# Optimization experiments

Measured on AMD Instinct MI355X. Metric: run time of the kernel, lower is better.

## Reference

```python
import jax, jax.numpy as jnp
import numpy as np

NUM_TYPES = 8
NUM_REL = 6
N_LAYERS = 2


def setup_inputs() -> dict:
    key = jax.random.key(0)
    ks = jax.random.split(key, 8)
    N, E, D_in, D = 20000, 320000, 512, 256
    node_feature = jax.random.normal(ks[0], (N, D_in), dtype=jnp.float32)
    node_type = jax.random.randint(ks[1], (N,), 0, NUM_TYPES)
    edge_index = jax.random.randint(ks[2], (2, E), 0, N)
    edge_type = jax.random.randint(ks[3], (E,), 0, NUM_REL)
    node_position = jnp.arange(N)
    # learned params
    adapt_W = jax.random.normal(ks[4], (NUM_TYPES, D, D_in), dtype=jnp.float32) * 0.02
    adapt_b = jnp.zeros((NUM_TYPES, D), dtype=jnp.float32)
    W_rel = jax.random.normal(ks[5], (N_LAYERS, NUM_REL, D, D), dtype=jnp.float32) * 0.05
    W_self = jax.random.normal(ks[6], (N_LAYERS, D, D), dtype=jnp.float32) * 0.05
    b_self = jnp.zeros((N_LAYERS, D), dtype=jnp.float32)
    return {
        "node_feature": node_feature,
        "node_type": node_type,
        "edge_index": edge_index,
        "edge_type": edge_type,
        "node_position": node_position,
        "adapt_W": adapt_W,
        "adapt_b": adapt_b,
        "W_rel": W_rel,
        "W_self": W_self,
        "b_self": b_self,
    }


def reference(node_feature, node_type, edge_index, edge_type, node_position,
              adapt_W, adapt_b, W_rel, W_self, b_self):
    N = node_feature.shape[0]
    D = adapt_W.shape[1]
    # per-node-type adaptation: res[i] = tanh(W_{t_i} x_i + b_{t_i})
    # (original loops over types with boolean gather/scatter; here we mask-select)
    h = jnp.zeros((N, D), dtype=node_feature.dtype)
    for t in range(NUM_TYPES):
        y = jnp.tanh(node_feature @ adapt_W[t].T + adapt_b[t])
        h = jnp.where((node_type == t)[:, None], y, h)
    # dropout p=0.0 -> identity
    src, dst = edge_index[0], edge_index[1]
    deg = jax.ops.segment_sum(jnp.ones(src.shape, h.dtype), dst, num_segments=N)
    inv_deg = (1.0 / jnp.maximum(deg, 1.0))[:, None]  # [N,1]
    # relational GNN layer stack (stand-in for unseen GraphConv)
    for l in range(N_LAYERS):
        hr = jnp.einsum('nd,rde->rne', h, W_rel[l])      # [R,N,D]
        msg = hr[edge_type, src]                          # [E,D] gather by (relation, src)
        agg = jax.ops.segment_sum(msg, dst, num_segments=N)
        h = jax.nn.relu(agg * inv_deg + h @ W_self[l] + b_self[l])
    return h
```

## Files before the change

kernel.cpp:

```cpp
#include <hip/hip_runtime.h>

constexpr int NTYPES = 8;
constexpr int NREL   = 6;
constexpr int NSLOT  = 7;
constexpr int D      = 256;
constexpr int DIN    = 512;
constexpr int LDH    = NSLOT * D;

using short8 = __attribute__((ext_vector_type(8))) short;
using f32x4  = __attribute__((ext_vector_type(4))) float;

__device__ __forceinline__ ushort f2b(float f) {
  unsigned u = __float_as_uint(f);
  u += 0x7fffu + ((u >> 16) & 1u);
  return (ushort)(u >> 16);
}
__device__ __forceinline__ float b2f(unsigned bits16) {
  return __uint_as_float(bits16 << 16);
}

#define GLOAD_LDS16(g, l)                                              \
  __builtin_amdgcn_global_load_lds(                                    \
      (__attribute__((address_space(1))) void*)(g),                    \
      (__attribute__((address_space(3))) void*)(l), 16, 0, 0)

__global__ void k_prep_fused(int* __restrict__ deg,
                             const float* __restrict__ X, ushort* __restrict__ Xb,
                             const float* __restrict__ Wa, ushort* __restrict__ Wab,
                             const float* __restrict__ Wrel, const float* __restrict__ Wself,
                             ushort* __restrict__ Wcat,
                             int N, int nz, int nx, int nw, int n4x, int n4w) {
  const int b = blockIdx.x;
  const int tid = threadIdx.x;
  if (b < nz) {
    int i = b * 256 + tid;
    if (i < N) deg[i] = 0;
  } else if (b < nz + nx) {
    int i = (b - nz) * 256 + tid;
    if (i < n4x) {
      float4 v = ((const float4*)X)[i];
      ushort4 o; o.x = f2b(v.x); o.y = f2b(v.y); o.z = f2b(v.z); o.w = f2b(v.w);
      ((ushort4*)Xb)[i] = o;
    }
  } else if (b < nz + nx + nw) {
    int i = (b - nz - nx) * 256 + tid;
    if (i < n4w) {
      float4 v = ((const float4*)Wa)[i];
      ushort4 o; o.x = f2b(v.x); o.y = f2b(v.y); o.z = f2b(v.z); o.w = f2b(v.w);
      ((ushort4*)Wab)[i] = o;
    }
  } else {
    int local = b - nz - nx - nw;
    int l = local / (NSLOT * 256);
    int s = (local % (NSLOT * 256)) / 256;
    int o = (local % 256) * 256 + tid;
    int e = o >> 8, d = o & 255;
    float v = (s < NREL) ? Wrel[(((size_t)l * NREL + s) * D + d) * D + e]
                         : Wself[((size_t)l * D + d) * D + e];
    Wcat[(((size_t)l * NSLOT + s) * D + e) * D + d] = f2b(v);
  }
}

__global__ void k_count_fused(const int* __restrict__ ntype, int* __restrict__ blockcnt,
                              const int* __restrict__ dst, int* __restrict__ deg,
                              int N, int E, int nbN) {
  __shared__ int cnt[NTYPES];
  const int b = blockIdx.x;
  if (b < nbN) {
    int i = b * 256 + threadIdx.x;
    if (threadIdx.x < NTYPES) cnt[threadIdx.x] = 0;
    __syncthreads();
    int t = (i < N) ? ntype[i] : -1;
#pragma unroll
    for (int ty = 0; ty < NTYPES; ++ty) {
      unsigned long long m = __ballot(t == ty);
      if ((threadIdx.x & 63) == 0 && m) atomicAdd(&cnt[ty], __popcll(m));
    }
    __syncthreads();
    if (threadIdx.x < NTYPES) blockcnt[b * NTYPES + threadIdx.x] = cnt[threadIdx.x];
  } else {
    int e = (b - nbN) * 256 + threadIdx.x;
    if (e < E) atomicAdd(&deg[dst[e]], 1);
  }
}

__global__ __launch_bounds__(512)
void k_type_scan(const int* __restrict__ blockcnt, int* __restrict__ boffset,
                 int* __restrict__ cnt, int* __restrict__ offt, int nb) {
  __shared__ int tot[NTYPES];
  __shared__ int base[NTYPES];
  const int w = threadIdx.x >> 6;
  const int l = threadIdx.x & 63;
  int v0 = (l < nb) ? blockcnt[l * NTYPES + w] : 0;
  int v1 = (64 + l < nb) ? blockcnt[(64 + l) * NTYPES + w] : 0;
  int s0 = v0;
#pragma unroll
  for (int o = 1; o < 64; o <<= 1) { int t = __shfl_up(s0, o); if (l >= o) s0 += t; }
  int total0 = __shfl(s0, 63);
  int s1 = v1;
#pragma unroll
  for (int o = 1; o < 64; o <<= 1) { int t = __shfl_up(s1, o); if (l >= o) s1 += t; }
  s1 += total0;
  int totalw = __shfl(s1, 63);
  if (l == 0) { tot[w] = totalw; cnt[w] = totalw; }
  __syncthreads();
  if (threadIdx.x == 0) {
    int s = 0;
    for (int ty = 0; ty < NTYPES; ++ty) { base[ty] = s; offt[ty] = s; s += tot[ty]; }
  }
  __syncthreads();
  const int bs = base[w];
  if (l < nb) boffset[l * NTYPES + w] = bs + s0 - v0;
  if (64 + l < nb) boffset[(64 + l) * NTYPES + w] = bs + s1 - v1;
}

__global__ void k_scatter_scan(const int* __restrict__ ntype, const int* __restrict__ boffset,
                               int* __restrict__ perm,
                               const int* __restrict__ deg, int* __restrict__ rowptr,
                               int* __restrict__ bsum, int N, int nbN) {
  __shared__ int sm[256];
  const int b = blockIdx.x;
  if (b < nbN) {
    int i = b * 256 + threadIdx.x;
    if (threadIdx.x < NTYPES) sm[threadIdx.x] = boffset[b * NTYPES + threadIdx.x];
    __syncthreads();
    int t = (i < N) ? ntype[i] : -1;
    int lane = threadIdx.x & 63;
#pragma unroll
    for (int ty = 0; ty < NTYPES; ++ty) {
      unsigned long long m = __ballot(t == ty);
      if (m) {
        int wbase = 0;
        if (lane == 0) wbase = atomicAdd(&sm[ty], __popcll(m));
        wbase = __shfl(wbase, 0);
        if (t == ty) {
          int rank = __popcll(m & ((1ull << lane) - 1ull));
          perm[wbase + rank] = i;
        }
      }
    }
  } else {
    const int bb = b - nbN;
    int i = bb * 256 + threadIdx.x;
    int v = (i < N) ? deg[i] : 0;
    sm[threadIdx.x] = v;
    __syncthreads();
    for (int o = 1; o < 256; o <<= 1) {
      int t = (threadIdx.x >= o) ? sm[threadIdx.x - o] : 0;
      __syncthreads();
      sm[threadIdx.x] += t;
      __syncthreads();
    }
    if (i < N) rowptr[i] = sm[threadIdx.x] - v;
    if (threadIdx.x == 255) bsum[bb] = sm[255];
  }
}

__global__ __launch_bounds__(64)
void k_scan_bsum(int* __restrict__ bsum, int nb) {
  const int l = threadIdx.x;
  int v0 = (l < nb) ? bsum[l] : 0;
  int v1 = (64 + l < nb) ? bsum[64 + l] : 0;
  int s0 = v0;
#pragma unroll
  for (int o = 1; o < 64; o <<= 1) { int t = __shfl_up(s0, o); if (l >= o) s0 += t; }
  int total0 = __shfl(s0, 63);
  int s1 = v1;
#pragma unroll
  for (int o = 1; o < 64; o <<= 1) { int t = __shfl_up(s1, o); if (l >= o) s1 += t; }
  s1 += total0;
  if (l < nb) bsum[l] = s0 - v0;
  if (64 + l < nb) bsum[64 + l] = s1 - v1;
}

__global__ void k_scan_add(int* __restrict__ rowptr, int* __restrict__ cursor,
                           const int* __restrict__ bsum, const int* __restrict__ deg,
                           float* __restrict__ inv, int N, int E) {
  int i = blockIdx.x * 256 + threadIdx.x;
  if (i < N) {
    int r = rowptr[i] + bsum[blockIdx.x];
    rowptr[i] = r;
    cursor[i] = r;
    inv[i] = 1.0f / fmaxf((float)deg[i], 1.0f);
  }
  if (i == 0) rowptr[N] = E;
}
__global__ void k_sortedges(const int* __restrict__ src, const int* __restrict__ dst,
                            const int* __restrict__ et, int* cursor,
                            int* __restrict__ epack, int E) {
  int e = blockIdx.x * 256 + threadIdx.x;
  if (e < E) {
    int pos = atomicAdd(&cursor[dst[e]], 1);
    epack[pos] = (src[e] << 3) | et[e];
  }
}

template <int BM, int BN, int NTN, int KDIM, bool ADAPT, int OCC>
__global__ __launch_bounds__(256, OCC)
void k_mfma_gemm(const ushort* __restrict__ A, const ushort* __restrict__ B,
                 const float* __restrict__ bias,
                 const int* __restrict__ perm, const int* __restrict__ cnt,
                 const int* __restrict__ off,
                 ushort* __restrict__ Cout, int N, int ldC) {
  const int nwg = gridDim.x;
  const int qq = nwg >> 3, rr = nwg & 7;
  const int xcd = blockIdx.x & 7, idx = blockIdx.x >> 3;
  const int wgid = (xcd < rr ? xcd * (qq + 1) : rr * (qq + 1) + (xcd - rr) * qq) + idx;

  int mcnt = N, mtile, ntile;
  const int* permt = nullptr;
  const ushort* Bt = B;
  const float* biast = bias;
  if (ADAPT) {
    const int mt = nwg / (NTYPES * NTN);
    const int t = wgid / (mt * NTN);
    const int rem = wgid % (mt * NTN);
    mtile = rem / NTN;
    ntile = rem % NTN;
    mcnt = cnt[t];
    permt = perm + off[t];
    Bt = B + (size_t)t * D * KDIM;
    biast = bias + t * D;
  } else {
    mtile = wgid / NTN;
    ntile = wgid % NTN;
  }
  const int m0 = mtile * BM;
  if (m0 >= mcnt) return;
  const int n0 = ntile * BN;

  __shared__ ushort SM[3][2][BM * 32];
  static_assert(BM * BN <= 3 * 2 * BM * 32, "C tile must fit in staging LDS");

  const int tid  = threadIdx.x;
  const int lane = tid & 63;
  const int w    = tid >> 6;
  constexpr int FR = BM / 32;
  constexpr int FC = BN / 32;
  const int wr   = (w >> 1) * (BM / 2);
  const int wc   = (w & 1) * (BN / 2);

  constexpr int PW = BM / 16 / 4;
  const ushort* gA[PW];
  const ushort* gB[PW];
  int lo[PW];
#pragma unroll
  for (int u = 0; u < PW; ++u) {
    const int c  = w + u * 4;
    const int r  = c * 16 + (lane >> 2);
    const int sl = (lane & 3) ^ ((r >> 1) & 3);
    int ga;
    if (ADAPT) ga = permt[min(m0 + r, mcnt - 1)];
    else       ga = min(m0 + r, N - 1);
    gA[u] = A + (size_t)ga * KDIM + sl * 8;
    gB[u] = Bt + (size_t)(n0 + r) * KDIM + sl * 8;
    lo[u] = c * 512;
  }

  auto STAGE = [&](int k0, int buf) {
#pragma unroll
    for (int u = 0; u < PW; ++u) {
      GLOAD_LDS16(gA[u] + k0, &SM[buf][0][lo[u]]);
      GLOAD_LDS16(gB[u] + k0, &SM[buf][1][lo[u]]);
    }
  };
  auto WAIT_LPS = [&]() {
    if constexpr (PW == 1) asm volatile("s_waitcnt vmcnt(2)" ::: "memory");
    else                   asm volatile("s_waitcnt vmcnt(4)" ::: "memory");
  };

  f32x4 acc[FR][FC] = {};
  const int r15 = lane & 15;
  const int g   = lane >> 4;
  const int gsw = g ^ ((r15 >> 1) & 3);

  auto COMPUTE = [&](int buf) {
    short8 af[FR], bf[FC];
#pragma unroll
    for (int i = 0; i < FR; ++i)
      af[i] = *(const short8*)(&SM[buf][0][(wr + i * 16 + r15) * 32 + gsw * 8]);
#pragma unroll
    for (int j = 0; j < FC; ++j)
      bf[j] = *(const short8*)(&SM[buf][1][(wc + j * 16 + r15) * 32 + gsw * 8]);
#pragma unroll
    for (int i = 0; i < FR; ++i)
#pragma unroll
      for (int j = 0; j < FC; ++j)
        acc[i][j] = __builtin_amdgcn_mfma_f32_16x16x32_bf16(af[i], bf[j], acc[i][j], 0, 0, 0);
  };

  constexpr int NT = KDIM / 32;
  static_assert(NT >= 3, "pipeline needs NT >= 3");

  STAGE(0, 0);
  STAGE(32, 1);

#pragma unroll
  for (int kt = 0; kt < NT - 1; ++kt) {
    WAIT_LPS();
    __builtin_amdgcn_s_barrier();
    __builtin_amdgcn_sched_barrier(0);
    COMPUTE(kt % 3);
    if (kt + 2 < NT) STAGE((kt + 2) * 32, (kt + 2) % 3);
  }
  asm volatile("s_waitcnt vmcnt(0)" ::: "memory");
  __builtin_amdgcn_s_barrier();
  __builtin_amdgcn_sched_barrier(0);
  COMPUTE((NT - 1) % 3);

  __syncthreads();
  ushort* Ct = (ushort*)SM;
#pragma unroll
  for (int i = 0; i < FR; ++i) {
#pragma unroll
    for (int q4 = 0; q4 < 4; ++q4) {
      const int row = wr + i * 16 + (lane >> 4) * 4 + q4;
#pragma unroll
      for (int j = 0; j < FC; ++j) {
        const int col = wc + j * 16 + r15;
        float v = acc[i][j][q4];
        if (ADAPT) v = tanhf(v + biast[n0 + col]);
        Ct[row * BN + col] = f2b(v);
      }
    }
  }
  __syncthreads();
  constexpr int C8 = BN / 8;
  constexpr int UNITS = BM * C8;
#pragma unroll
  for (int u0 = 0; u0 < UNITS; u0 += 256) {
    const int u = u0 + tid;
    const int row = u / C8, c8 = u % C8;
    const int rl = m0 + row;
    if (rl < mcnt) {
      const int grow = ADAPT ? permt[rl] : rl;
      *(short8*)(Cout + (size_t)grow * ldC + n0 + c8 * 8) =
          *(const short8*)(Ct + row * BN + c8 * 8);
    }
  }
}

template <bool LAST>
__global__ void k_combine(const ushort* __restrict__ Hall, const int* __restrict__ rowptr,
                          const int* __restrict__ epack, const float* __restrict__ invd,
                          const float* __restrict__ bias, void* __restrict__ outp, int N) {
  int v = blockIdx.x * 4 + (threadIdx.x >> 6);
  if (v >= N) return;
  int lane = threadIdx.x & 63;
  int e0 = rowptr[v], e1 = rowptr[v + 1];
  const uint2 s = *(const uint2*)(Hall + (size_t)v * LDH + NREL * D + lane * 4);
  float iv = invd[v];
  const float4 b4 = *(const float4*)(bias + lane * 4);

  float a0 = 0.f, a1 = 0.f, a2 = 0.f, a3 = 0.f;
  int e = e0;
  for (; e + 8 <= e1; e += 8) {
    uint2 u[8];
#pragma unroll
    for (int k = 0; k < 8; ++k) {
      int p = epack[e + k];
      u[k] = *(const uint2*)(Hall + (size_t)(p >> 3) * LDH + (p & 7) * D + lane * 4);
    }
#pragma unroll
    for (int k = 0; k < 8; ++k) {
      a0 += b2f(u[k].x & 0xffffu);
      a1 += __uint_as_float(u[k].x & 0xffff0000u);
      a2 += b2f(u[k].y & 0xffffu);
      a3 += __uint_as_float(u[k].y & 0xffff0000u);
    }
  }
  if (e + 4 <= e1) {
    uint2 u[4];
#pragma unroll
    for (int k = 0; k < 4; ++k) {
      int p = epack[e + k];
      u[k] = *(const uint2*)(Hall + (size_t)(p >> 3) * LDH + (p & 7) * D + lane * 4);
    }
#pragma unroll
    for (int k = 0; k < 4; ++k) {
      a0 += b2f(u[k].x & 0xffffu);
      a1 += __uint_as_float(u[k].x & 0xffff0000u);
      a2 += b2f(u[k].y & 0xffffu);
      a3 += __uint_as_float(u[k].y & 0xffff0000u);
    }
    e += 4;
  }
  for (; e < e1; ++e) {
    int p = epack[e];
    const uint2 u = *(const uint2*)(Hall + (size_t)(p >> 3) * LDH + (p & 7) * D + lane * 4);
    a0 += b2f(u.x & 0xffffu);
    a1 += __uint_as_float(u.x & 0xffff0000u);
    a2 += b2f(u.y & 0xffffu);
    a3 += __uint_as_float(u.y & 0xffff0000u);
  }
  float o0 = fmaxf(fmaf(a0, iv, b2f(s.x & 0xffffu)) + b4.x, 0.f);
  float o1 = fmaxf(fmaf(a1, iv, __uint_as_float(s.x & 0xffff0000u)) + b4.y, 0.f);
  float o2 = fmaxf(fmaf(a2, iv, b2f(s.y & 0xffffu)) + b4.z, 0.f);
  float o3 = fmaxf(fmaf(a3, iv, __uint_as_float(s.y & 0xffff0000u)) + b4.w, 0.f);
  if (LAST) {
    float4 o; o.x = o0; o.y = o1; o.z = o2; o.w = o3;
    ((float4*)outp)[(size_t)v * 64 + lane] = o;
  } else {
    ushort4 o; o.x = f2b(o0); o.y = f2b(o1); o.z = f2b(o2); o.w = f2b(o3);
    ((ushort4*)outp)[(size_t)v * 64 + lane] = o;
  }
}

extern "C" void kernel_launch(void* const* d_in, const int* in_sizes, int n_in,
                              void* d_out, int out_size, void* d_ws, size_t ws_size,
                              hipStream_t stream) {
  const float* X       = (const float*)d_in[0];
  const int*   ntype   = (const int*)d_in[1];
  const int*   eidx    = (const int*)d_in[2];
  const int*   etype   = (const int*)d_in[3];
  const float* adapt_W = (const float*)d_in[5];
  const float* adapt_b = (const float*)d_in[6];
  const float* W_rel   = (const float*)d_in[7];
  const float* W_self  = (const float*)d_in[8];
  const float* b_self  = (const float*)d_in[9];

  const int N = in_sizes[1];
  const int E = in_sizes[3];
  const int* src = eidx;
  const int* dst = eidx + E;

  char* ws = (char*)d_ws;
  size_t o = 0;
  auto alloc = [&](size_t bytes) { void* p = ws + o; o += (bytes + 255) & ~255ull; return p; };

  ushort* Hall  = (ushort*)alloc((size_t)N * LDH * 2);
  ushort* Xb    = Hall;
  ushort* h     = (ushort*)alloc((size_t)N * D * 2);
  ushort* Wab   = (ushort*)alloc((size_t)NTYPES * D * DIN * 2);
  ushort* Wcat  = (ushort*)alloc((size_t)2 * NSLOT * D * D * 2);
  int*   deg    = (int*)alloc((size_t)N * 4);
  float* inv    = (float*)alloc((size_t)N * 4);
  int*   perm   = (int*)alloc((size_t)N * 4);
  int*   rowptr = (int*)alloc((size_t)(N + 1) * 4);
  int*   cursor = (int*)alloc((size_t)N * 4);
  int*   epack  = (int*)alloc((size_t)E * 4);
  int*   bsum   = (int*)alloc(1024 * 4);
  int*   blockcnt = (int*)alloc((size_t)1024 * NTYPES * 4);
  int*   boffset  = (int*)alloc((size_t)1024 * NTYPES * 4);
  int*   cnt    = (int*)alloc(NTYPES * 4);
  int*   offt   = (int*)alloc(NTYPES * 4);

  const int thr = 256;
  const int nbN = (N + thr - 1) / thr;
  const int nbE = (E + thr - 1) / thr;

  const int n4x = N * DIN / 4;
  const int n4w = NTYPES * D * DIN / 4;
  const int nz = nbN;
  const int nx = (n4x + thr - 1) / thr;
  const int nw = (n4w + thr - 1) / thr;
  const int np = 2 * NSLOT * (D * D / 256);
  k_prep_fused<<<nz + nx + nw + np, thr, 0, stream>>>(deg, X, Xb, adapt_W, Wab,
                                                      W_rel, W_self, Wcat,
                                                      N, nz, nx, nw, n4x, n4w);

  k_count_fused<<<nbN + nbE, thr, 0, stream>>>(ntype, blockcnt, dst, deg, N, E, nbN);
  k_type_scan<<<1, 512, 0, stream>>>(blockcnt, boffset, cnt, offt, nbN);
  k_scatter_scan<<<2 * nbN, thr, 0, stream>>>(ntype, boffset, perm, deg, rowptr, bsum, N, nbN);
  k_scan_bsum<<<1, 64, 0, stream>>>(bsum, nbN);
  k_scan_add<<<nbN, 256, 0, stream>>>(rowptr, cursor, bsum, deg, inv, N, E);
  k_sortedges<<<nbE, 256, 0, stream>>>(src, dst, etype, cursor, epack, E);

  const int mtA = (N + 63) / 64;
  const int nwgA = NTYPES * mtA * (D / 64);
  k_mfma_gemm<64, 64, D / 64, DIN, true, 6><<<nwgA, 256, 0, stream>>>(
      Xb, Wab, adapt_b, perm, cnt, offt, h, N, D);

  const int mtL = (N + 127) / 128;
  const int nwgL = mtL * (LDH / 128);
  for (int l = 0; l < 2; ++l) {
    const ushort* Wl = Wcat + (size_t)l * NSLOT * D * D;
    k_mfma_gemm<128, 128, LDH / 128, D, false, 4><<<nwgL, 256, 0, stream>>>(
        h, Wl, nullptr, nullptr, nullptr, nullptr, Hall, N, LDH);
    if (l == 0)
      k_combine<false><<<(N + 3) / 4, 256, 0, stream>>>(Hall, rowptr, epack, inv,
                                                        b_self + (size_t)l * D, h, N);
    else
      k_combine<true><<<(N + 3) / 4, 256, 0, stream>>>(Hall, rowptr, epack, inv,
                                                       b_self + (size_t)l * D, d_out, N);
  }
}
```

Baseline: 191.5 us.

## Merge preprocessing kernels and fold edge sort into adaptation GEMM launch

Cuts the preprocessing chain from seven launches to five. Type counting and degree atomics move into the conversion kernel, the type scan and a 512-wide degree scan share one launch, and the block-sum scan rides on the scatter kernel. The edge bucketing runs as extra blocks appended to the adaptation GEMM grid, so it overlaps with the matrix work. The GEMM now takes its tile count as an argument, and a separate zeroing kernel resets the degree counts before the fused kernel. The point is to remove launch gaps and serial dependencies between small kernels, at the cost of mixing atomic-heavy blocks into the GEMM grid.

New measurement: 187.5 us, median of 4. -2.0%, faster.

```diff
diff --git a/kernel.cpp b/kernel.cpp
--- a/kernel.cpp
+++ b/kernel.cpp
@@ -24,33 +24,38 @@
       (__attribute__((address_space(1))) void*)(g),                    \
       (__attribute__((address_space(3))) void*)(l), 16, 0, 0)
 
-__global__ void k_prep_fused(int* __restrict__ deg,
-                             const float* __restrict__ X, ushort* __restrict__ Xb,
-                             const float* __restrict__ Wa, ushort* __restrict__ Wab,
-                             const float* __restrict__ Wrel, const float* __restrict__ Wself,
-                             ushort* __restrict__ Wcat,
-                             int N, int nz, int nx, int nw, int n4x, int n4w) {
+__global__ void k_zero(int* __restrict__ p, int n) {
+  int i = blockIdx.x * blockDim.x + threadIdx.x;
+  if (i < n) p[i] = 0;
+}
+
+__global__ void k_prep_mega(const float* __restrict__ X, ushort* __restrict__ Xb,
+                            const float* __restrict__ Wa, ushort* __restrict__ Wab,
+                            const float* __restrict__ Wrel, const float* __restrict__ Wself,
+                            ushort* __restrict__ Wcat,
+                            const int* __restrict__ ntype, int* __restrict__ blockcnt,
+                            const int* __restrict__ dst, int* __restrict__ deg,
+                            int N, int E, int nx, int nw, int np, int nbN,
+                            int n4x, int n4w) {
+  __shared__ int cnt[NTYPES];
   const int b = blockIdx.x;
   const int tid = threadIdx.x;
-  if (b < nz) {
+  if (b < nx) {
     int i = b * 256 + tid;
-    if (i < N) deg[i] = 0;
-  } else if (b < nz + nx) {
-    int i = (b - nz) * 256 + tid;
     if (i < n4x) {
       float4 v = ((const float4*)X)[i];
       ushort4 o; o.x = f2b(v.x); o.y = f2b(v.y); o.z = f2b(v.z); o.w = f2b(v.w);
       ((ushort4*)Xb)[i] = o;
     }
-  } else if (b < nz + nx + nw) {
-    int i = (b - nz - nx) * 256 + tid;
+  } else if (b < nx + nw) {
+    int i = (b - nx) * 256 + tid;
     if (i < n4w) {
       float4 v = ((const float4*)Wa)[i];
       ushort4 o; o.x = f2b(v.x); o.y = f2b(v.y); o.z = f2b(v.z); o.w = f2b(v.w);
       ((ushort4*)Wab)[i] = o;
     }
-  } else {
-    int local = b - nz - nx - nw;
+  } else if (b < nx + nw + np) {
+    int local = b - nx - nw;
     int l = local / (NSLOT * 256);
     int s = (local % (NSLOT * 256)) / 256;
     int o = (local % 256) * 256 + tid;
@@ -58,71 +63,83 @@
     float v = (s < NREL) ? Wrel[(((size_t)l * NREL + s) * D + d) * D + e]
                          : Wself[((size_t)l * D + d) * D + e];
     Wcat[(((size_t)l * NSLOT + s) * D + e) * D + d] = f2b(v);
-  }
-}
-
-__global__ void k_count_fused(const int* __restrict__ ntype, int* __restrict__ blockcnt,
-                              const int* __restrict__ dst, int* __restrict__ deg,
-                              int N, int E, int nbN) {
-  __shared__ int cnt[NTYPES];
+  } else if (b < nx + nw + np + nbN) {
+    const int bb = b - nx - nw - np;
+    int i = bb * 256 + tid;
+    if (tid < NTYPES) cnt[tid] = 0;
+    __syncthreads();
+    int t = (i < N) ? ntype[i] : -1;
+#pragma unroll
+    for (int ty = 0; ty < NTYPES; ++ty) {
+      unsigned long long m = __ballot(t == ty);
+      if ((tid & 63) == 0 && m) atomicAdd(&cnt[ty], __popcll(m));
+    }
+    __syncthreads();
+    if (tid < NTYPES) blockcnt[bb * NTYPES + tid] = cnt[tid];
+  } else {
+    int e = (b - nx - nw - np - nbN) * 256 + tid;
+    if (e < E) atomicAdd(&deg[dst[e]], 1);
+  }
+}
+
+__global__ __launch_bounds__(512)
+void k_scan2(const int* __restrict__ blockcnt, int* __restrict__ boffset,
+             int* __restrict__ cnt, int* __restrict__ offt, int nbN,
+             const int* __restrict__ deg, int* __restrict__ rowptr,
+             int* __restrict__ bsum, int N) {
+  if (blockIdx.x == 0) {
+    __shared__ int tot[NTYPES];
+    __shared__ int base[NTYPES];
+    const int w = threadIdx.x >> 6;
+    const int l = threadIdx.x & 63;
+    int v0 = (l < nbN) ? blockcnt[l * NTYPES + w] : 0;
+    int v1 = (64 + l < nbN) ? blockcnt[(64 + l) * NTYPES + w] : 0;
+    int s0 = v0;
+#pragma unroll
+    for (int o = 1; o < 64; o <<= 1) { int t = __shfl_up(s0, o); if (l >= o) s0 += t; }
+    int total0 = __shfl(s0, 63);
+    int s1 = v1;
+#pragma unroll
+    for (int o = 1; o < 64; o <<= 1) { int t = __shfl_up(s1, o); if (l >= o) s1 += t; }
+    s1 += total0;
+    int totalw = __shfl(s1, 63);
+    if (l == 0) { tot[w] = totalw; cnt[w] = totalw; }
+    __syncthreads();
+    if (threadIdx.x == 0) {
+      int s = 0;
+      for (int ty = 0; ty < NTYPES; ++ty) { base[ty] = s; offt[ty] = s; s += tot[ty]; }
+    }
+    __syncthreads();
+    const int bs = base[w];
+    if (l < nbN) boffset[l * NTYPES + w] = bs + s0 - v0;
+    if (64 + l < nbN) boffset[(64 + l) * NTYPES + w] = bs + s1 - v1;
+  } else {
+    __shared__ int sm[512];
+    const int bb = blockIdx.x - 1;
+    const int t = threadIdx.x;
+    int i = bb * 512 + t;
+    int v = (i < N) ? deg[i] : 0;
+    sm[t] = v;
+    __syncthreads();
+    for (int o = 1; o < 512; o <<= 1) {
+      int x = (t >= o) ? sm[t - o] : 0;
+      __syncthreads();
+      sm[t] += x;
+      __syncthreads();
+    }
+    if (i < N) rowptr[i] = sm[t] - v;
+    if (t == 511) bsum[bb] = sm[511];
+  }
+}
+
+__global__ void k_scatter_bsum(const int* __restrict__ ntype, const int* __restrict__ boffset,
+                               int* __restrict__ perm, int N, int nbN,
+                               int* __restrict__ bsum, int nbs) {
+  __shared__ int cur[NTYPES];
   const int b = blockIdx.x;
   if (b < nbN) {
     int i = b * 256 + threadIdx.x;
-    if (threadIdx.x < NTYPES) cnt[threadIdx.x] = 0;
-    __syncthreads();
-    int t = (i < N) ? ntype[i] : -1;
-#pragma unroll
-    for (int ty = 0; ty < NTYPES; ++ty) {
-      unsigned long long m = __ballot(t == ty);
-      if ((threadIdx.x & 63) == 0 && m) atomicAdd(&cnt[ty], __popcll(m));
-    }
-    __syncthreads();
-    if (threadIdx.x < NTYPES) blockcnt[b * NTYPES + threadIdx.x] = cnt[threadIdx.x];
-  } else {
-    int e = (b - nbN) * 256 + threadIdx.x;
-    if (e < E) atomicAdd(&deg[dst[e]], 1);
-  }
-}
-
-__global__ __launch_bounds__(512)
-void k_type_scan(const int* __restrict__ blockcnt, int* __restrict__ boffset,
-                 int* __restrict__ cnt, int* __restrict__ offt, int nb) {
-  __shared__ int tot[NTYPES];
-  __shared__ int base[NTYPES];
-  const int w = threadIdx.x >> 6;
-  const int l = threadIdx.x & 63;
-  int v0 = (l < nb) ? blockcnt[l * NTYPES + w] : 0;
-  int v1 = (64 + l < nb) ? blockcnt[(64 + l) * NTYPES + w] : 0;
-  int s0 = v0;
-#pragma unroll
-  for (int o = 1; o < 64; o <<= 1) { int t = __shfl_up(s0, o); if (l >= o) s0 += t; }
-  int total0 = __shfl(s0, 63);
-  int s1 = v1;
-#pragma unroll
-  for (int o = 1; o < 64; o <<= 1) { int t = __shfl_up(s1, o); if (l >= o) s1 += t; }
-  s1 += total0;
-  int totalw = __shfl(s1, 63);
-  if (l == 0) { tot[w] = totalw; cnt[w] = totalw; }
-  __syncthreads();
-  if (threadIdx.x == 0) {
-    int s = 0;
-    for (int ty = 0; ty < NTYPES; ++ty) { base[ty] = s; offt[ty] = s; s += tot[ty]; }
-  }
-  __syncthreads();
-  const int bs = base[w];
-  if (l < nb) boffset[l * NTYPES + w] = bs + s0 - v0;
-  if (64 + l < nb) boffset[(64 + l) * NTYPES + w] = bs + s1 - v1;
-}
-
-__global__ void k_scatter_scan(const int* __restrict__ ntype, const int* __restrict__ boffset,
-                               int* __restrict__ perm,
-                               const int* __restrict__ deg, int* __restrict__ rowptr,
-                               int* __restrict__ bsum, int N, int nbN) {
-  __shared__ int sm[256];
-  const int b = blockIdx.x;
-  if (b < nbN) {
-    int i = b * 256 + threadIdx.x;
-    if (threadIdx.x < NTYPES) sm[threadIdx.x] = boffset[b * NTYPES + threadIdx.x];
+    if (threadIdx.x < NTYPES) cur[threadIdx.x] = boffset[b * NTYPES + threadIdx.x];
     __syncthreads();
     int t = (i < N) ? ntype[i] : -1;
     int lane = threadIdx.x & 63;
@@ -131,7 +148,7 @@
       unsigned long long m = __ballot(t == ty);
       if (m) {
         int wbase = 0;
-        if (lane == 0) wbase = atomicAdd(&sm[ty], __popcll(m));
+        if (lane == 0) wbase = atomicAdd(&cur[ty], __popcll(m));
         wbase = __shfl(wbase, 0);
         if (t == ty) {
           int rank = __popcll(m & ((1ull << lane) - 1ull));
@@ -139,38 +156,14 @@
         }
       }
     }
-  } else {
-    const int bb = b - nbN;
-    int i = bb * 256 + threadIdx.x;
-    int v = (i < N) ? deg[i] : 0;
-    sm[threadIdx.x] = v;
-    __syncthreads();
-    for (int o = 1; o < 256; o <<= 1) {
-      int t = (threadIdx.x >= o) ? sm[threadIdx.x - o] : 0;
-      __syncthreads();
-      sm[threadIdx.x] += t;
-      __syncthreads();
-    }
-    if (i < N) rowptr[i] = sm[threadIdx.x] - v;
-    if (threadIdx.x == 255) bsum[bb] = sm[255];
-  }
-}
-
-__global__ __launch_bounds__(64)
-void k_scan_bsum(int* __restrict__ bsum, int nb) {
-  const int l = threadIdx.x;
-  int v0 = (l < nb) ? bsum[l] : 0;
-  int v1 = (64 + l < nb) ? bsum[64 + l] : 0;
-  int s0 = v0;
-#pragma unroll
-  for (int o = 1; o < 64; o <<= 1) { int t = __shfl_up(s0, o); if (l >= o) s0 += t; }
-  int total0 = __shfl(s0, 63);
-  int s1 = v1;
-#pragma unroll
-  for (int o = 1; o < 64; o <<= 1) { int t = __shfl_up(s1, o); if (l >= o) s1 += t; }
-  s1 += total0;
-  if (l < nb) bsum[l] = s0 - v0;
-  if (64 + l < nb) bsum[64 + l] = s1 - v1;
+  } else if (threadIdx.x < 64) {
+    const int l = threadIdx.x;
+    int v0 = (l < nbs) ? bsum[l] : 0;
+    int s0 = v0;
+#pragma unroll
+    for (int o = 1; o < 64; o <<= 1) { int t = __shfl_up(s0, o); if (l >= o) s0 += t; }
+    if (l < nbs) bsum[l] = s0 - v0;
+  }
 }
 
 __global__ void k_scan_add(int* __restrict__ rowptr, int* __restrict__ cursor,
@@ -178,31 +171,33 @@
                            float* __restrict__ inv, int N, int E) {
   int i = blockIdx.x * 256 + threadIdx.x;
   if (i < N) {
-    int r = rowptr[i] + bsum[blockIdx.x];
+    int r = rowptr[i] + bsum[i >> 9];
     rowptr[i] = r;
     cursor[i] = r;
     inv[i] = 1.0f / fmaxf((float)deg[i], 1.0f);
   }
   if (i == 0) rowptr[N] = E;
 }
-__global__ void k_sortedges(const int* __restrict__ src, const int* __restrict__ dst,
-                            const int* __restrict__ et, int* cursor,
-                            int* __restrict__ epack, int E) {
-  int e = blockIdx.x * 256 + threadIdx.x;
-  if (e < E) {
-    int pos = atomicAdd(&cursor[dst[e]], 1);
-    epack[pos] = (src[e] << 3) | et[e];
-  }
-}
-
-template <int BM, int BN, int NTN, int KDIM, bool ADAPT, int OCC>
+
+template <int BM, int BN, int NTN, int KDIM, bool ADAPT, bool SORT, int OCC>
 __global__ __launch_bounds__(256, OCC)
 void k_mfma_gemm(const ushort* __restrict__ A, const ushort* __restrict__ B,
                  const float* __restrict__ bias,
                  const int* __restrict__ perm, const int* __restrict__ cnt,
                  const int* __restrict__ off,
-                 ushort* __restrict__ Cout, int N, int ldC) {
-  const int nwg = gridDim.x;
+                 ushort* __restrict__ Cout, int N, int ldC, int nwg,
+                 const int* __restrict__ s_src, const int* __restrict__ s_dst,
+                 const int* __restrict__ s_et, int* __restrict__ s_cursor,
+                 int* __restrict__ s_epack, int s_E) {
+  if (SORT && (int)blockIdx.x >= nwg) {
+    int e = ((int)blockIdx.x - nwg) * 256 + threadIdx.x;
+    if (e < s_E) {
+      int pos = atomicAdd(&s_cursor[s_dst[e]], 1);
+      s_epack[pos] = (s_src[e] << 3) | s_et[e];
+    }
+    return;
+  }
+
   const int qq = nwg >> 3, rr = nwg & 7;
   const int xcd = blockIdx.x & 7, idx = blockIdx.x >> 3;
   const int wgid = (xcd < rr ? xcd * (qq + 1) : rr * (qq + 1) + (xcd - rr) * qq) + idx;
@@ -448,35 +443,39 @@
   const int thr = 256;
   const int nbN = (N + thr - 1) / thr;
   const int nbE = (E + thr - 1) / thr;
+  const int nbN512 = (N + 511) / 512;
+
+  k_zero<<<nbN, thr, 0, stream>>>(deg, N);
 
   const int n4x = N * DIN / 4;
   const int n4w = NTYPES * D * DIN / 4;
-  const int nz = nbN;
   const int nx = (n4x + thr - 1) / thr;
   const int nw = (n4w + thr - 1) / thr;
   const int np = 2 * NSLOT * (D * D / 256);
-  k_prep_fused<<<nz + nx + nw + np, thr, 0, stream>>>(deg, X, Xb, adapt_W, Wab,
-                                                      W_rel, W_self, Wcat,
-                                                      N, nz, nx, nw, n4x, n4w);
-
-  k_count_fused<<<nbN + nbE, thr, 0, stream>>>(ntype, blockcnt, dst, deg, N, E, nbN);
-  k_type_scan<<<1, 512, 0, stream>>>(blockcnt, boffset, cnt, offt, nbN);
-  k_scatter_scan<<<2 * nbN, thr, 0, stream>>>(ntype, boffset, perm, deg, rowptr, bsum, N, nbN);
-  k_scan_bsum<<<1, 64, 0, stream>>>(bsum, nbN);
-  k_scan_add<<<nbN, 256, 0, stream>>>(rowptr, cursor, bsum, deg, inv, N, E);
-  k_sortedges<<<nbE, 256, 0, stream>>>(src, dst, etype, cursor, epack, E);
+  k_prep_mega<<<nx + nw + np + nbN + nbE, thr, 0, stream>>>(
+      X, Xb, adapt_W, Wab, W_rel, W_self, Wcat, ntype, blockcnt, dst, deg,
+      N, E, nx, nw, np, nbN, n4x, n4w);
+
+  k_scan2<<<1 + nbN512, 512, 0, stream>>>(blockcnt, boffset, cnt, offt, nbN,
+                                          deg, rowptr, bsum, N);
+
+  k_scatter_bsum<<<nbN + 1, thr, 0, stream>>>(ntype, boffset, perm, N, nbN, bsum, nbN512);
+
+  k_scan_add<<<nbN, thr, 0, stream>>>(rowptr, cursor, bsum, deg, inv, N, E);
 
   const int mtA = (N + 63) / 64;
   const int nwgA = NTYPES * mtA * (D / 64);
-  k_mfma_gemm<64, 64, D / 64, DIN, true, 6><<<nwgA, 256, 0, stream>>>(
-      Xb, Wab, adapt_b, perm, cnt, offt, h, N, D);
+  k_mfma_gemm<64, 64, D / 64, DIN, true, true, 6><<<nwgA + nbE, 256, 0, stream>>>(
+      Xb, Wab, adapt_b, perm, cnt, offt, h, N, D, nwgA,
+      src, dst, etype, cursor, epack, E);
 
   const int mtL = (N + 127) / 128;
   const int nwgL = mtL * (LDH / 128);
   for (int l = 0; l < 2; ++l) {
     const ushort* Wl = Wcat + (size_t)l * NSLOT * D * D;
-    k_mfma_gemm<128, 128, LDH / 128, D, false, 4><<<nwgL, 256, 0, stream>>>(
-        h, Wl, nullptr, nullptr, nullptr, nullptr, Hall, N, LDH);
+    k_mfma_gemm<128, 128, LDH / 128, D, false, false, 4><<<nwgL, 256, 0, stream>>>(
+        h, Wl, nullptr, nullptr, nullptr, nullptr, Hall, N, LDH, nwgL,
+        nullptr, nullptr, nullptr, nullptr, nullptr, 0);
     if (l == 0)
       k_combine<false><<<(N + 3) / 4, 256, 0, stream>>>(Hall, rowptr, epack, inv,
                                                         b_self + (size_t)l * D, h, N);
```
